# Performance work log

Hardware: AMD Instinct MI355X
Metric: run time of the kernel (lower is better)

Reference implementation:

```python
import jax, jax.numpy as jnp
import numpy as np

C_IN = 2048
N_EXP = 64
TOPK = 2


def setup_inputs() -> dict:
    key = jax.random.key(0)
    kx, kw, kb = jax.random.split(key, 3)
    x = jax.random.normal(kx, (4, 4096, C_IN), dtype=jnp.float32)
    # nn.Linear(c_in, n_exp): weight [n_exp, c_in], bias [n_exp]
    bound = 1.0 / np.sqrt(C_IN)
    W = jax.random.uniform(kw, (N_EXP, C_IN), minval=-bound, maxval=bound, dtype=jnp.float32)
    b = jax.random.uniform(kb, (N_EXP,), minval=-bound, maxval=bound, dtype=jnp.float32)
    return {"x": x, "W": W, "b": b}


def reference(x, W, b):
    # linear: [B,S,C] @ [C,E] + [E] -> [B,S,E]
    logits = jnp.einsum("bsc,ec->bse", x, W) + b
    probs = jax.nn.softmax(logits, axis=-1)
    vals, idx = jax.lax.top_k(probs, TOPK)  # [B,S,K]
    # scatter top-k values back to full expert dim; other entries zero
    onehot = jax.nn.one_hot(idx, N_EXP, dtype=probs.dtype)  # [B,S,K,E]
    gate_out = jnp.einsum("bsk,bske->bse", vals, onehot)
    return gate_out
```

## Files before the change

kernel.cpp:

```cpp
#include <hip/hip_runtime.h>
#include <math.h>

#define C_IN 2048
#define N_EXP 64
#define TPB 16
#define KWIN 512
#define KSTEPS 16
#define DELTA  3e-4f
#define DELTA2 1e-3f

typedef __bf16 bf16x8 __attribute__((ext_vector_type(8)));
typedef float f32x4 __attribute__((ext_vector_type(4)));

__device__ __forceinline__ void cvt_split(float f, ushort& h, ushort& l) {
    uint u = __float_as_uint(f);
    uint hr = (u + (0x7FFFu + ((u >> 16) & 1u))) >> 16;
    h = (ushort)hr;
    float hf = __uint_as_float(hr << 16);
    uint v = __float_as_uint(f - hf);
    l = (ushort)((v + (0x7FFFu + ((v >> 16) & 1u))) >> 16);
}

__global__ void conv_w_kernel(const float* __restrict__ W,
                              ushort* __restrict__ whf, ushort* __restrict__ wlf) {
    const int o = blockIdx.x * 256 + threadIdx.x;
    const int egks = o >> 9;
    const int lane = (o >> 3) & 63;
    const int j = o & 7;
    const int e = (egks >> 6) * 16 + (lane & 15);
    const int k = (egks & 63) * 32 + (lane >> 4) * 8 + j;
    ushort h, lo;
    cvt_split(W[e * C_IN + k], h, lo);
    whf[o] = h;
    wlf[o] = lo;
}

__global__ __launch_bounds__(256, 4) void topk_gate_kernel(
    const float* __restrict__ x, const float* __restrict__ Wf,
    const float* __restrict__ b, const ushort* __restrict__ whf,
    const ushort* __restrict__ wlf, float* __restrict__ out)
{
    __shared__ float part[4][TPB][65];

    const int tid = threadIdx.x;
    const int wv = tid >> 6, l = tid & 63;
    const int t0 = blockIdx.x * TPB;
    const int tr = l & 15;
    const int kg = l >> 4;

    const float* xg = x + (size_t)(t0 + tr) * C_IN + wv * KWIN + kg * 8;

    f32x4 acc[4];
#pragma unroll
    for (int eg = 0; eg < 4; ++eg) acc[eg] = (f32x4){0.f, 0.f, 0.f, 0.f};

#pragma unroll 2
    for (int ks = 0; ks < KSTEPS; ++ks) {
        const float4 a0 = *(const float4*)(xg + ks * 32);
        const float4 a1 = *(const float4*)(xg + ks * 32 + 4);
        const int ksa = wv * KSTEPS + ks;
        uint4 wb[8];
#pragma unroll
        for (int eg = 0; eg < 4; ++eg) {
            wb[eg * 2 + 0] = *(const uint4*)&whf[(eg * 64 + ksa) * 512 + l * 8];
            wb[eg * 2 + 1] = *(const uint4*)&wlf[(eg * 64 + ksa) * 512 + l * 8];
        }
        ushort h[8], q[8];
        cvt_split(a0.x, h[0], q[0]); cvt_split(a0.y, h[1], q[1]);
        cvt_split(a0.z, h[2], q[2]); cvt_split(a0.w, h[3], q[3]);
        cvt_split(a1.x, h[4], q[4]); cvt_split(a1.y, h[5], q[5]);
        cvt_split(a1.z, h[6], q[6]); cvt_split(a1.w, h[7], q[7]);
        uint4 hv = {(uint)h[0] | ((uint)h[1] << 16), (uint)h[2] | ((uint)h[3] << 16),
                    (uint)h[4] | ((uint)h[5] << 16), (uint)h[6] | ((uint)h[7] << 16)};
        uint4 qv = {(uint)q[0] | ((uint)q[1] << 16), (uint)q[2] | ((uint)q[3] << 16),
                    (uint)q[4] | ((uint)q[5] << 16), (uint)q[6] | ((uint)q[7] << 16)};
        bf16x8 ah = __builtin_bit_cast(bf16x8, hv);
        bf16x8 al = __builtin_bit_cast(bf16x8, qv);
#pragma unroll
        for (int eg = 0; eg < 4; ++eg) {
            bf16x8 bh = __builtin_bit_cast(bf16x8, wb[eg * 2 + 0]);
            bf16x8 bl = __builtin_bit_cast(bf16x8, wb[eg * 2 + 1]);
            acc[eg] = __builtin_amdgcn_mfma_f32_16x16x32_bf16(ah, bh, acc[eg], 0, 0, 0);
            acc[eg] = __builtin_amdgcn_mfma_f32_16x16x32_bf16(al, bh, acc[eg], 0, 0, 0);
            acc[eg] = __builtin_amdgcn_mfma_f32_16x16x32_bf16(ah, bl, acc[eg], 0, 0, 0);
        }
    }

#pragma unroll
    for (int eg = 0; eg < 4; ++eg)
#pragma unroll
    for (int r = 0; r < 4; ++r)
        part[wv][kg * 4 + r][eg * 16 + tr] = acc[eg][r];
    __syncthreads();

    const int e = l;
    const float be = b[e];
    for (int ti = 0; ti < 4; ++ti) {
        const int t = wv * 4 + ti;
        float logit = part[0][t][e] + part[1][t][e]
                    + part[2][t][e] + part[3][t][e] + be;

        float v1, v2, v3; int i1, i2;
        for (int pass = 0; pass < 2; ++pass) {
            v1 = logit; i1 = e;
#pragma unroll
            for (int off = 32; off >= 1; off >>= 1) {
                float ov = __shfl_xor(v1, off, 64);
                int   oi = __shfl_xor(i1, off, 64);
                if (ov > v1 || (ov == v1 && oi < i1)) { v1 = ov; i1 = oi; }
            }
            v2 = (e == i1) ? -3.4e38f : logit;
            i2 = (e == i1) ? N_EXP : e;
#pragma unroll
            for (int off = 32; off >= 1; off >>= 1) {
                float ov = __shfl_xor(v2, off, 64);
                int   oi = __shfl_xor(i2, off, 64);
                if (ov > v2 || (ov == v2 && oi < i2)) { v2 = ov; i2 = oi; }
            }
            v3 = (e == i1 || e == i2) ? -3.4e38f : logit;
#pragma unroll
            for (int off = 32; off >= 1; off >>= 1) {
                float ov = __shfl_xor(v3, off, 64);
                v3 = (ov > v3) ? ov : v3;
            }
            if (pass == 1) break;
            const bool risky = (v1 - v2 < DELTA) || (v2 - v3 < DELTA);
            if (!risky) break;
            unsigned long long cm = __ballot(logit >= v2 - DELTA2);
            const float* xr = x + (size_t)(t0 + t) * C_IN;
            while (cm) {
                const int ce = __ffsll((unsigned long long)cm) - 1;
                cm &= cm - 1;
                const float* wr = Wf + (size_t)ce * C_IN;
                float p = 0.f;
#pragma unroll 8
                for (int i = 0; i < 32; ++i)
                    p = fmaf(xr[l + 64 * i], wr[l + 64 * i], p);
#pragma unroll
                for (int off = 32; off >= 1; off >>= 1)
                    p += __shfl_xor(p, off, 64);
                if (e == ce) logit = p + be;
            }
        }

        float ex = expf(logit - v1);
        float ssum = ex;
#pragma unroll
        for (int off = 32; off >= 1; off >>= 1)
            ssum += __shfl_xor(ssum, off, 64);
        const float inv = 1.0f / ssum;
        const float p1 = inv;
        const float p2 = expf(v2 - v1) * inv;
        const float o = (e == i1) ? p1 : ((e == i2) ? p2 : 0.0f);
        out[(size_t)(t0 + t) * N_EXP + e] = o;
    }
}

extern "C" void kernel_launch(void* const* d_in, const int* in_sizes, int n_in,
                              void* d_out, int out_size, void* d_ws, size_t ws_size,
                              hipStream_t stream) {
    const float* x = (const float*)d_in[0];
    const float* W = (const float*)d_in[1];
    const float* b = (const float*)d_in[2];
    float* out = (float*)d_out;

    ushort* whf = (ushort*)d_ws;
    ushort* wlf = whf + N_EXP * C_IN;

    conv_w_kernel<<<512, 256, 0, stream>>>(W, whf, wlf);

    const int tokens = in_sizes[0] / C_IN;
    const int grid = tokens / TPB;
    topk_gate_kernel<<<grid, 256, 0, stream>>>(x, W, b, whf, wlf, out);
}
```

Baseline: 56.47 us.

## Double-buffer weight tiles via async global-to-LDS loads and process 32 tokens per block

Each block now handles 32 tokens as two 16-row MFMA fragments, so every weight fragment loaded is reused across twice as many tokens. Weight tiles are streamed into double-buffered LDS with global_load_lds while the next x chunk is prefetched into registers, and explicit vmcnt waits overlap loads with the MFMA work. MFMA issue priority is raised around the compute section. This lowers weight traffic per token and hides load latency, at the cost of 64KB of LDS per block, lower occupancy (launch bounds 2) and half as many blocks.

```diff
diff --git a/kernel.cpp b/kernel.cpp
--- a/kernel.cpp
+++ b/kernel.cpp
@@ -3,8 +3,7 @@
 
 #define C_IN 2048
 #define N_EXP 64
-#define TPB 16
-#define KWIN 512
+#define TPB 32
 #define KSTEPS 16
 #define DELTA  3e-4f
 #define DELTA2 1e-3f
@@ -35,70 +34,131 @@
     wlf[o] = lo;
 }
 
-__global__ __launch_bounds__(256, 4) void topk_gate_kernel(
+__device__ __forceinline__ void gload16(const ushort* g, ushort* l) {
+    __builtin_amdgcn_global_load_lds(
+        (const __attribute__((address_space(1))) uint32_t*)g,
+        (__attribute__((address_space(3))) uint32_t*)l, 16, 0, 0);
+}
+
+__global__ __launch_bounds__(256, 2) void topk_gate_kernel(
     const float* __restrict__ x, const float* __restrict__ Wf,
     const float* __restrict__ b, const ushort* __restrict__ whf,
     const ushort* __restrict__ wlf, float* __restrict__ out)
 {
-    __shared__ float part[4][TPB][65];
+    __shared__ __align__(16) ushort smem[32768];
 
     const int tid = threadIdx.x;
-    const int wv = tid >> 6, l = tid & 63;
+    const int w = tid >> 6, l = tid & 63;
     const int t0 = blockIdx.x * TPB;
     const int tr = l & 15;
     const int kg = l >> 4;
 
-    const float* xg = x + (size_t)(t0 + tr) * C_IN + wv * KWIN + kg * 8;
-
-    f32x4 acc[4];
-#pragma unroll
-    for (int eg = 0; eg < 4; ++eg) acc[eg] = (f32x4){0.f, 0.f, 0.f, 0.f};
-
-#pragma unroll 2
-    for (int ks = 0; ks < KSTEPS; ++ks) {
-        const float4 a0 = *(const float4*)(xg + ks * 32);
-        const float4 a1 = *(const float4*)(xg + ks * 32 + 4);
-        const int ksa = wv * KSTEPS + ks;
-        uint4 wb[8];
+    ushort* wbase = smem + w * 8192;
+
+    const float* xg = x + (size_t)t0 * C_IN + w * (KSTEPS * 32) + kg * 8;
+
+    f32x4 acc[2][4];
+#pragma unroll
+    for (int mf = 0; mf < 2; ++mf)
+#pragma unroll
+    for (int eg = 0; eg < 4; ++eg) acc[mf][eg] = (f32x4){0.f, 0.f, 0.f, 0.f};
+
+#define WSTAGE(I) do {                                                        \
+    const int ksa_ = w * KSTEPS + (I);                                        \
+    ushort* dst_ = wbase + ((I) & 1) * 4096;                                  \
+    _Pragma("unroll") for (int eg_ = 0; eg_ < 4; ++eg_) {                     \
+        gload16(whf + (size_t)(eg_ * 64 + ksa_) * 512 + l * 8,                \
+                dst_ + (eg_ * 2 + 0) * 512 + l * 8);                          \
+        gload16(wlf + (size_t)(eg_ * 64 + ksa_) * 512 + l * 8,                \
+                dst_ + (eg_ * 2 + 1) * 512 + l * 8);                          \
+    } } while (0)
+
+#define XLOAD(DST, I) do {                                                    \
+    (DST)[0] = *(const float4*)(xg + (size_t)tr * C_IN + (I) * 32);           \
+    (DST)[1] = *(const float4*)(xg + (size_t)tr * C_IN + (I) * 32 + 4);       \
+    (DST)[2] = *(const float4*)(xg + (size_t)(tr + 16) * C_IN + (I) * 32);    \
+    (DST)[3] = *(const float4*)(xg + (size_t)(tr + 16) * C_IN + (I) * 32 + 4);\
+    } while (0)
+
+    float4 xb[2][4];
+    WSTAGE(0);
+    XLOAD(xb[0], 0);
+
+#pragma unroll
+    for (int i = 0; i < KSTEPS; ++i) {
+        if (i + 1 < KSTEPS) {
+            WSTAGE(i + 1);
+            XLOAD(xb[(i + 1) & 1], i + 1);
+            asm volatile("s_waitcnt vmcnt(12)" ::: "memory");
+        } else {
+            asm volatile("s_waitcnt vmcnt(0)" ::: "memory");
+        }
+        __builtin_amdgcn_sched_barrier(0);
+
+        const ushort* tb = wbase + (i & 1) * 4096;
+        uint4 bfr[8];
 #pragma unroll
         for (int eg = 0; eg < 4; ++eg) {
-            wb[eg * 2 + 0] = *(const uint4*)&whf[(eg * 64 + ksa) * 512 + l * 8];
-            wb[eg * 2 + 1] = *(const uint4*)&wlf[(eg * 64 + ksa) * 512 + l * 8];
-        }
-        ushort h[8], q[8];
-        cvt_split(a0.x, h[0], q[0]); cvt_split(a0.y, h[1], q[1]);
-        cvt_split(a0.z, h[2], q[2]); cvt_split(a0.w, h[3], q[3]);
-        cvt_split(a1.x, h[4], q[4]); cvt_split(a1.y, h[5], q[5]);
-        cvt_split(a1.z, h[6], q[6]); cvt_split(a1.w, h[7], q[7]);
-        uint4 hv = {(uint)h[0] | ((uint)h[1] << 16), (uint)h[2] | ((uint)h[3] << 16),
+            bfr[eg * 2 + 0] = *(const uint4*)&tb[(eg * 2 + 0) * 512 + l * 8];
+            bfr[eg * 2 + 1] = *(const uint4*)&tb[(eg * 2 + 1) * 512 + l * 8];
+        }
+
+        const float4* xc = xb[i & 1];
+        ushort h[16], q[16];
+        cvt_split(xc[0].x, h[0], q[0]); cvt_split(xc[0].y, h[1], q[1]);
+        cvt_split(xc[0].z, h[2], q[2]); cvt_split(xc[0].w, h[3], q[3]);
+        cvt_split(xc[1].x, h[4], q[4]); cvt_split(xc[1].y, h[5], q[5]);
+        cvt_split(xc[1].z, h[6], q[6]); cvt_split(xc[1].w, h[7], q[7]);
+        cvt_split(xc[2].x, h[8], q[8]); cvt_split(xc[2].y, h[9], q[9]);
+        cvt_split(xc[2].z, h[10], q[10]); cvt_split(xc[2].w, h[11], q[11]);
+        cvt_split(xc[3].x, h[12], q[12]); cvt_split(xc[3].y, h[13], q[13]);
+        cvt_split(xc[3].z, h[14], q[14]); cvt_split(xc[3].w, h[15], q[15]);
+        uint4 h0 = {(uint)h[0] | ((uint)h[1] << 16), (uint)h[2] | ((uint)h[3] << 16),
                     (uint)h[4] | ((uint)h[5] << 16), (uint)h[6] | ((uint)h[7] << 16)};
-        uint4 qv = {(uint)q[0] | ((uint)q[1] << 16), (uint)q[2] | ((uint)q[3] << 16),
+        uint4 q0 = {(uint)q[0] | ((uint)q[1] << 16), (uint)q[2] | ((uint)q[3] << 16),
                     (uint)q[4] | ((uint)q[5] << 16), (uint)q[6] | ((uint)q[7] << 16)};
-        bf16x8 ah = __builtin_bit_cast(bf16x8, hv);
-        bf16x8 al = __builtin_bit_cast(bf16x8, qv);
+        uint4 h1 = {(uint)h[8] | ((uint)h[9] << 16), (uint)h[10] | ((uint)h[11] << 16),
+                    (uint)h[12] | ((uint)h[13] << 16), (uint)h[14] | ((uint)h[15] << 16)};
+        uint4 q1 = {(uint)q[8] | ((uint)q[9] << 16), (uint)q[10] | ((uint)q[11] << 16),
+                    (uint)q[12] | ((uint)q[13] << 16), (uint)q[14] | ((uint)q[15] << 16)};
+        bf16x8 ah0 = __builtin_bit_cast(bf16x8, h0);
+        bf16x8 al0 = __builtin_bit_cast(bf16x8, q0);
+        bf16x8 ah1 = __builtin_bit_cast(bf16x8, h1);
+        bf16x8 al1 = __builtin_bit_cast(bf16x8, q1);
+
+        __builtin_amdgcn_s_setprio(1);
 #pragma unroll
         for (int eg = 0; eg < 4; ++eg) {
-            bf16x8 bh = __builtin_bit_cast(bf16x8, wb[eg * 2 + 0]);
-            bf16x8 bl = __builtin_bit_cast(bf16x8, wb[eg * 2 + 1]);
-            acc[eg] = __builtin_amdgcn_mfma_f32_16x16x32_bf16(ah, bh, acc[eg], 0, 0, 0);
-            acc[eg] = __builtin_amdgcn_mfma_f32_16x16x32_bf16(al, bh, acc[eg], 0, 0, 0);
-            acc[eg] = __builtin_amdgcn_mfma_f32_16x16x32_bf16(ah, bl, acc[eg], 0, 0, 0);
-        }
+            bf16x8 bh = __builtin_bit_cast(bf16x8, bfr[eg * 2 + 0]);
+            bf16x8 bl = __builtin_bit_cast(bf16x8, bfr[eg * 2 + 1]);
+            acc[0][eg] = __builtin_amdgcn_mfma_f32_16x16x32_bf16(ah0, bh, acc[0][eg], 0, 0, 0);
+            acc[1][eg] = __builtin_amdgcn_mfma_f32_16x16x32_bf16(ah1, bh, acc[1][eg], 0, 0, 0);
+            acc[0][eg] = __builtin_amdgcn_mfma_f32_16x16x32_bf16(al0, bh, acc[0][eg], 0, 0, 0);
+            acc[1][eg] = __builtin_amdgcn_mfma_f32_16x16x32_bf16(al1, bh, acc[1][eg], 0, 0, 0);
+            acc[0][eg] = __builtin_amdgcn_mfma_f32_16x16x32_bf16(ah0, bl, acc[0][eg], 0, 0, 0);
+            acc[1][eg] = __builtin_amdgcn_mfma_f32_16x16x32_bf16(ah1, bl, acc[1][eg], 0, 0, 0);
+        }
+        __builtin_amdgcn_s_setprio(0);
     }
 
+    float* pw = (float*)wbase;
+#pragma unroll
+    for (int mf = 0; mf < 2; ++mf)
 #pragma unroll
     for (int eg = 0; eg < 4; ++eg)
 #pragma unroll
     for (int r = 0; r < 4; ++r)
-        part[wv][kg * 4 + r][eg * 16 + tr] = acc[eg][r];
+        pw[(mf * 16 + kg * 4 + r) * 64 + eg * 16 + tr] = acc[mf][eg][r];
+
     __syncthreads();
 
+    const float* fp = (const float*)smem;
     const int e = l;
     const float be = b[e];
-    for (int ti = 0; ti < 4; ++ti) {
-        const int t = wv * 4 + ti;
-        float logit = part[0][t][e] + part[1][t][e]
-                    + part[2][t][e] + part[3][t][e] + be;
+    for (int ti = 0; ti < 8; ++ti) {
+        const int t = w * 8 + ti;
+        float logit = fp[0 * 4096 + t * 64 + e] + fp[1 * 4096 + t * 64 + e]
+                    + fp[2 * 4096 + t * 64 + e] + fp[3 * 4096 + t * 64 + e] + be;
 
         float v1, v2, v3; int i1, i2;
         for (int pass = 0; pass < 2; ++pass) {
@@ -154,6 +214,8 @@
         const float o = (e == i1) ? p1 : ((e == i2) ? p2 : 0.0f);
         out[(size_t)(t0 + t) * N_EXP + e] = o;
     }
+#undef WSTAGE
+#undef XLOAD
 }
 
 extern "C" void kernel_launch(void* const* d_in, const int* in_sizes, int n_in,
```

After: 54.59 us. -3.3%, faster.

## Stage weight and activation chunks through LDS with a 4-deep async pipeline

Applied to the files above, without the earlier changes.

Rewrites the gate GEMM so each block handles 32 tokens and the four waves split the expert dimension instead of K. Weight chunks are streamed into LDS with global_load_lds, and x chunks are converted to bf16 hi/lo once per block into LDS, both in a 4-stage ring with explicit vmcnt waits and barriers. This removes the cross-wave K-reduction and cuts redundant per-wave weight loads, in exchange for more barriers, lower occupancy (launch bounds 2) and fragile hand-tuned wait counts.

```diff
diff --git a/kernel.cpp b/kernel.cpp
--- a/kernel.cpp
+++ b/kernel.cpp
@@ -3,9 +3,8 @@
 
 #define C_IN 2048
 #define N_EXP 64
-#define TPB 16
-#define KWIN 512
-#define KSTEPS 16
+#define TPB 32
+#define NCH 64
 #define DELTA  3e-4f
 #define DELTA2 1e-3f
 
@@ -22,83 +21,143 @@
 }
 
 __global__ void conv_w_kernel(const float* __restrict__ W,
-                              ushort* __restrict__ whf, ushort* __restrict__ wlf) {
-    const int o = blockIdx.x * 256 + threadIdx.x;
-    const int egks = o >> 9;
-    const int lane = (o >> 3) & 63;
-    const int j = o & 7;
-    const int e = (egks >> 6) * 16 + (lane & 15);
-    const int k = (egks & 63) * 32 + (lane >> 4) * 8 + j;
+                              ushort* __restrict__ whc, ushort* __restrict__ wlc) {
+    const int i = blockIdx.x * 256 + threadIdx.x;
+    const int e = i >> 11, k = i & 2047;
+    const int o = (k >> 5) * 2048 + e * 32 + (k & 31);
     ushort h, lo;
-    cvt_split(W[e * C_IN + k], h, lo);
-    whf[o] = h;
-    wlf[o] = lo;
-}
-
-__global__ __launch_bounds__(256, 4) void topk_gate_kernel(
+    cvt_split(W[i], h, lo);
+    whc[o] = h;
+    wlc[o] = lo;
+}
+
+__device__ __forceinline__ void glds16(const ushort* g, ushort* l) {
+    __builtin_amdgcn_global_load_lds(
+        (const __attribute__((address_space(1))) uint32_t*)g,
+        (__attribute__((address_space(3))) uint32_t*)l, 16, 0, 0);
+}
+
+#define VMW(N) do { asm volatile("s_waitcnt vmcnt(" #N ")" ::: "memory");     \
+                    __builtin_amdgcn_sched_barrier(0); } while (0)
+
+#define CVTW(XV, S2) do {                                                     \
+    ushort h0_, h1_, h2_, h3_, q0_, q1_, q2_, q3_;                            \
+    cvt_split((XV).x, h0_, q0_); cvt_split((XV).y, h1_, q1_);                 \
+    cvt_split((XV).z, h2_, q2_); cvt_split((XV).w, h3_, q3_);                 \
+    uint2 hv_ = {(uint)h0_ | ((uint)h1_ << 16), (uint)h2_ | ((uint)h3_ << 16)}; \
+    uint2 lv_ = {(uint)q0_ | ((uint)q1_ << 16), (uint)q2_ | ((uint)q3_ << 16)}; \
+    *(uint2*)&smem[16384 + (S2) * 2048 + xw] = hv_;                           \
+    *(uint2*)&smem[16384 + (S2) * 2048 + 1024 + xw] = lv_;                    \
+} while (0)
+
+#define KSTEP(u, W1, STG, CVT, W2) do {                                       \
+    VMW(W1);                                                                  \
+    __builtin_amdgcn_s_barrier();                                             \
+    const ushort* xs_ = smem + 16384 + (u) * 2048;                            \
+    const ushort* ws_ = smem + (u) * 4096;                                    \
+    uint4 rah0 = *(const uint4*)&xs_[aoff];                                   \
+    uint4 rah1 = *(const uint4*)&xs_[512 + aoff];                             \
+    uint4 ral0 = *(const uint4*)&xs_[1024 + aoff];                            \
+    uint4 ral1 = *(const uint4*)&xs_[1536 + aoff];                            \
+    uint4 rbh  = *(const uint4*)&ws_[boff];                                   \
+    uint4 rbl  = *(const uint4*)&ws_[2048 + boff];                            \
+    asm volatile("s_waitcnt lgkmcnt(0)" ::: "memory");                        \
+    __builtin_amdgcn_sched_barrier(0);                                        \
+    __builtin_amdgcn_s_barrier();                                             \
+    if (STG) {                                                                \
+        const int c4_ = cc + (u) + 4;                                         \
+        glds16(whc + (size_t)c4_ * 2048 + tid * 8,                            \
+               smem + (u) * 4096 + wavebase);                                 \
+        glds16(wlc + (size_t)c4_ * 2048 + tid * 8,                            \
+               smem + (u) * 4096 + 2048 + wavebase);                          \
+        xr[u] = *(const float4*)(xg + (size_t)xrow * C_IN + c4_ * 32 + xq * 4); \
+        __builtin_amdgcn_sched_barrier(0);                                    \
+    }                                                                         \
+    __builtin_amdgcn_s_setprio(1);                                            \
+    {                                                                         \
+        bf16x8 ah0 = __builtin_bit_cast(bf16x8, rah0);                        \
+        bf16x8 ah1 = __builtin_bit_cast(bf16x8, rah1);                        \
+        bf16x8 al0 = __builtin_bit_cast(bf16x8, ral0);                        \
+        bf16x8 al1 = __builtin_bit_cast(bf16x8, ral1);                        \
+        bf16x8 bh = __builtin_bit_cast(bf16x8, rbh);                          \
+        bf16x8 bl = __builtin_bit_cast(bf16x8, rbl);                          \
+        acc0 = __builtin_amdgcn_mfma_f32_16x16x32_bf16(ah0, bh, acc0, 0, 0, 0); \
+        acc1 = __builtin_amdgcn_mfma_f32_16x16x32_bf16(ah1, bh, acc1, 0, 0, 0); \
+        acc0 = __builtin_amdgcn_mfma_f32_16x16x32_bf16(al0, bh, acc0, 0, 0, 0); \
+        acc1 = __builtin_amdgcn_mfma_f32_16x16x32_bf16(al1, bh, acc1, 0, 0, 0); \
+        acc0 = __builtin_amdgcn_mfma_f32_16x16x32_bf16(ah0, bl, acc0, 0, 0, 0); \
+        acc1 = __builtin_amdgcn_mfma_f32_16x16x32_bf16(ah1, bl, acc1, 0, 0, 0); \
+    }                                                                         \
+    __builtin_amdgcn_s_setprio(0);                                            \
+    if (CVT) {                                                                \
+        VMW(W2);                                                              \
+        CVTW(xr[((u) + 2) & 3], ((u) + 2) & 3);                               \
+    }                                                                         \
+} while (0)
+
+__global__ __launch_bounds__(256, 2) void topk_gate_kernel(
     const float* __restrict__ x, const float* __restrict__ Wf,
-    const float* __restrict__ b, const ushort* __restrict__ whf,
-    const ushort* __restrict__ wlf, float* __restrict__ out)
+    const float* __restrict__ b, const ushort* __restrict__ whc,
+    const ushort* __restrict__ wlc, float* __restrict__ out)
 {
-    __shared__ float part[4][TPB][65];
+    __shared__ __align__(16) ushort smem[24576];
 
     const int tid = threadIdx.x;
-    const int wv = tid >> 6, l = tid & 63;
+    const int w = tid >> 6, l = tid & 63;
+    const int tr = l & 15, kg = l >> 4;
+    const int xrow = tid >> 3, xq = tid & 7;
     const int t0 = blockIdx.x * TPB;
-    const int tr = l & 15;
-    const int kg = l >> 4;
-
-    const float* xg = x + (size_t)(t0 + tr) * C_IN + wv * KWIN + kg * 8;
-
-    f32x4 acc[4];
-#pragma unroll
-    for (int eg = 0; eg < 4; ++eg) acc[eg] = (f32x4){0.f, 0.f, 0.f, 0.f};
-
-#pragma unroll 2
-    for (int ks = 0; ks < KSTEPS; ++ks) {
-        const float4 a0 = *(const float4*)(xg + ks * 32);
-        const float4 a1 = *(const float4*)(xg + ks * 32 + 4);
-        const int ksa = wv * KSTEPS + ks;
-        uint4 wb[8];
-#pragma unroll
-        for (int eg = 0; eg < 4; ++eg) {
-            wb[eg * 2 + 0] = *(const uint4*)&whf[(eg * 64 + ksa) * 512 + l * 8];
-            wb[eg * 2 + 1] = *(const uint4*)&wlf[(eg * 64 + ksa) * 512 + l * 8];
-        }
-        ushort h[8], q[8];
-        cvt_split(a0.x, h[0], q[0]); cvt_split(a0.y, h[1], q[1]);
-        cvt_split(a0.z, h[2], q[2]); cvt_split(a0.w, h[3], q[3]);
-        cvt_split(a1.x, h[4], q[4]); cvt_split(a1.y, h[5], q[5]);
-        cvt_split(a1.z, h[6], q[6]); cvt_split(a1.w, h[7], q[7]);
-        uint4 hv = {(uint)h[0] | ((uint)h[1] << 16), (uint)h[2] | ((uint)h[3] << 16),
-                    (uint)h[4] | ((uint)h[5] << 16), (uint)h[6] | ((uint)h[7] << 16)};
-        uint4 qv = {(uint)q[0] | ((uint)q[1] << 16), (uint)q[2] | ((uint)q[3] << 16),
-                    (uint)q[4] | ((uint)q[5] << 16), (uint)q[6] | ((uint)q[7] << 16)};
-        bf16x8 ah = __builtin_bit_cast(bf16x8, hv);
-        bf16x8 al = __builtin_bit_cast(bf16x8, qv);
-#pragma unroll
-        for (int eg = 0; eg < 4; ++eg) {
-            bf16x8 bh = __builtin_bit_cast(bf16x8, wb[eg * 2 + 0]);
-            bf16x8 bl = __builtin_bit_cast(bf16x8, wb[eg * 2 + 1]);
-            acc[eg] = __builtin_amdgcn_mfma_f32_16x16x32_bf16(ah, bh, acc[eg], 0, 0, 0);
-            acc[eg] = __builtin_amdgcn_mfma_f32_16x16x32_bf16(al, bh, acc[eg], 0, 0, 0);
-            acc[eg] = __builtin_amdgcn_mfma_f32_16x16x32_bf16(ah, bl, acc[eg], 0, 0, 0);
-        }
-    }
-
-#pragma unroll
-    for (int eg = 0; eg < 4; ++eg)
-#pragma unroll
-    for (int r = 0; r < 4; ++r)
-        part[wv][kg * 4 + r][eg * 16 + tr] = acc[eg][r];
+    const int wavebase = w * 512;
+    const int aoff = tr * 32 + kg * 8;
+    const int boff = (w * 16 + tr) * 32 + kg * 8;
+    const int xw = xrow * 32 + xq * 4;
+
+    const float* xg = x + (size_t)t0 * C_IN;
+
+    f32x4 acc0 = {0.f, 0.f, 0.f, 0.f};
+    f32x4 acc1 = {0.f, 0.f, 0.f, 0.f};
+    float4 xr[4];
+
+#pragma unroll
+    for (int c0 = 0; c0 < 4; ++c0) {
+        glds16(whc + (size_t)c0 * 2048 + tid * 8, smem + c0 * 4096 + wavebase);
+        glds16(wlc + (size_t)c0 * 2048 + tid * 8, smem + c0 * 4096 + 2048 + wavebase);
+        xr[c0] = *(const float4*)(xg + (size_t)xrow * C_IN + c0 * 32 + xq * 4);
+        __builtin_amdgcn_sched_barrier(0);
+    }
+    VMW(6);
+    CVTW(xr[0], 0);
+    CVTW(xr[1], 1);
+    asm volatile("s_waitcnt lgkmcnt(0)" ::: "memory");
+    __builtin_amdgcn_sched_barrier(0);
+
+    int cc = 0;
+#pragma unroll 1
+    for (int j = 0; j < 15; ++j) {
+        KSTEP(0, 9, 1, 1, 6);
+        KSTEP(1, 9, 1, 1, 6);
+        KSTEP(2, 9, 1, 1, 6);
+        KSTEP(3, 9, 1, 1, 6);
+        cc += 4;
+    }
+    KSTEP(0, 9, 0, 1, 3);
+    KSTEP(1, 6, 0, 1, 0);
+    KSTEP(2, 3, 0, 0, 0);
+    KSTEP(3, 0, 0, 0, 0);
+
+    float* part = (float*)smem;
+#pragma unroll
+    for (int r = 0; r < 4; ++r) {
+        part[(kg * 4 + r) * 65 + w * 16 + tr] = acc0[r];
+        part[(16 + kg * 4 + r) * 65 + w * 16 + tr] = acc1[r];
+    }
     __syncthreads();
 
     const int e = l;
     const float be = b[e];
-    for (int ti = 0; ti < 4; ++ti) {
-        const int t = wv * 4 + ti;
-        float logit = part[0][t][e] + part[1][t][e]
-                    + part[2][t][e] + part[3][t][e] + be;
+    for (int ti = 0; ti < 8; ++ti) {
+        const int t = w * 8 + ti;
+        float logit = part[t * 65 + e] + be;
 
         float v1, v2, v3; int i1, i2;
         for (int pass = 0; pass < 2; ++pass) {
@@ -127,7 +186,7 @@
             const bool risky = (v1 - v2 < DELTA) || (v2 - v3 < DELTA);
             if (!risky) break;
             unsigned long long cm = __ballot(logit >= v2 - DELTA2);
-            const float* xr = x + (size_t)(t0 + t) * C_IN;
+            const float* xrp = x + (size_t)(t0 + t) * C_IN;
             while (cm) {
                 const int ce = __ffsll((unsigned long long)cm) - 1;
                 cm &= cm - 1;
@@ -135,7 +194,7 @@
                 float p = 0.f;
 #pragma unroll 8
                 for (int i = 0; i < 32; ++i)
-                    p = fmaf(xr[l + 64 * i], wr[l + 64 * i], p);
+                    p = fmaf(xrp[l + 64 * i], wr[l + 64 * i], p);
 #pragma unroll
                 for (int off = 32; off >= 1; off >>= 1)
                     p += __shfl_xor(p, off, 64);
@@ -164,12 +223,12 @@
     const float* b = (const float*)d_in[2];
     float* out = (float*)d_out;
 
-    ushort* whf = (ushort*)d_ws;
-    ushort* wlf = whf + N_EXP * C_IN;
-
-    conv_w_kernel<<<512, 256, 0, stream>>>(W, whf, wlf);
+    ushort* whc = (ushort*)d_ws;
+    ushort* wlc = whc + N_EXP * C_IN;
+
+    conv_w_kernel<<<512, 256, 0, stream>>>(W, whc, wlc);
 
     const int tokens = in_sizes[0] / C_IN;
     const int grid = tokens / TPB;
-    topk_gate_kernel<<<grid, 256, 0, stream>>>(x, W, b, whf, wlf, out);
-}
+    topk_gate_kernel<<<grid, 256, 0, stream>>>(x, W, b, whc, wlc, out);
+}
```

After: 66.03 us. 16.9% more time.

## Stage x and split weights through LDS with async global-to-LDS pipelining

Applied to the files above, without the earlier changes.

The GEMM is restructured so each block handles 32 tokens and each wave owns 16 experts across the full K dimension, instead of splitting K across waves and reducing partials afterwards. x tiles (swizzled) and per-wave weight fragments are streamed into LDS with global_load_lds, double/quad buffered, with explicit vmcnt waits and barriers. The goal is to overlap memory loads with MFMA work, share x across waves and drop the cross-wave partial reduction. In exchange, 64KB of LDS limits occupancy to 2 blocks per CU, and the hand-scheduled wait counts are fragile.

```diff
diff --git a/kernel.cpp b/kernel.cpp
--- a/kernel.cpp
+++ b/kernel.cpp
@@ -3,9 +3,8 @@
 
 #define C_IN 2048
 #define N_EXP 64
-#define TPB 16
-#define KWIN 512
-#define KSTEPS 16
+#define TPB 32
+#define NSC 16
 #define DELTA  3e-4f
 #define DELTA2 1e-3f
 
@@ -24,81 +23,156 @@
 __global__ void conv_w_kernel(const float* __restrict__ W,
                               ushort* __restrict__ whf, ushort* __restrict__ wlf) {
     const int o = blockIdx.x * 256 + threadIdx.x;
-    const int egks = o >> 9;
-    const int lane = (o >> 3) & 63;
+    const int wg = o >> 15;
+    const int ks = (o >> 9) & 63;
+    const int l = (o >> 3) & 63;
     const int j = o & 7;
-    const int e = (egks >> 6) * 16 + (lane & 15);
-    const int k = (egks & 63) * 32 + (lane >> 4) * 8 + j;
+    const int e = wg * 16 + (l & 15);
+    const int k = ks * 32 + (l >> 4) * 8 + j;
     ushort h, lo;
     cvt_split(W[e * C_IN + k], h, lo);
     whf[o] = h;
     wlf[o] = lo;
 }
 
-__global__ __launch_bounds__(256, 4) void topk_gate_kernel(
+__device__ __forceinline__ void glds16(const void* g, void* l) {
+    __builtin_amdgcn_global_load_lds(
+        (const __attribute__((address_space(1))) uint32_t*)g,
+        (__attribute__((address_space(3))) uint32_t*)l, 16, 0, 0);
+}
+
+__device__ __forceinline__ void cvt8(const float4 a, const float4 b2,
+                                     uint4& hv, uint4& lv) {
+    ushort h[8], q[8];
+    cvt_split(a.x, h[0], q[0]);  cvt_split(a.y, h[1], q[1]);
+    cvt_split(a.z, h[2], q[2]);  cvt_split(a.w, h[3], q[3]);
+    cvt_split(b2.x, h[4], q[4]); cvt_split(b2.y, h[5], q[5]);
+    cvt_split(b2.z, h[6], q[6]); cvt_split(b2.w, h[7], q[7]);
+    hv = (uint4){(uint)h[0] | ((uint)h[1] << 16), (uint)h[2] | ((uint)h[3] << 16),
+                 (uint)h[4] | ((uint)h[5] << 16), (uint)h[6] | ((uint)h[7] << 16)};
+    lv = (uint4){(uint)q[0] | ((uint)q[1] << 16), (uint)q[2] | ((uint)q[3] << 16),
+                 (uint)q[4] | ((uint)q[5] << 16), (uint)q[6] | ((uint)q[7] << 16)};
+}
+
+#define VMW(N) do { asm volatile("s_waitcnt vmcnt(" #N ")" ::: "memory");     \
+                    __builtin_amdgcn_sched_barrier(0); } while (0)
+
+#define STAGEX(BB, SCN) do {                                                  \
+    char* xd_ = smem + (BB) * 16384;                                          \
+    _Pragma("unroll") for (int i_ = 0; i_ < 4; ++i_) {                        \
+        const int row0_ = w * 8 + 2 * i_;                                     \
+        const int r_ = row0_ + (l >> 5);                                      \
+        const int su_ = (l & 31) ^ ((r_ & 7) << 1);                           \
+        glds16((const float*)x + (size_t)(t0 + r_) * C_IN + (SCN) * 128 + su_ * 4, \
+               (float*)(xd_ + row0_ * 512));                                  \
+    }                                                                         \
+    __builtin_amdgcn_sched_barrier(0);                                        \
+} while (0)
+
+#define KSTEP(K, VMN, DOSTG) do {                                             \
+    if (DOSTG) {                                                              \
+        const int ksg2_ = sc4 + (K) + 2;                                      \
+        const size_t wo_ = ((size_t)(w * 64 + ksg2_)) * 512 + l * 8;          \
+        glds16(whf + wo_, wsl + (((K) + 2) & 3) * 2048);                      \
+        glds16(wlf + wo_, wsl + (((K) + 2) & 3) * 2048 + 1024);               \
+        __builtin_amdgcn_sched_barrier(0);                                    \
+    }                                                                         \
+    VMW(VMN);                                                                 \
+    {                                                                         \
+        const int uo_ = (((K) * 8 + kg2) ^ sw) * 16;                         \
+        float4 a0lo_ = *(const float4*)(xb + aoff0 + uo_);                    \
+        float4 a0hi_ = *(const float4*)(xb + aoff0 + uo_ + 16);               \
+        float4 a1lo_ = *(const float4*)(xb + aoff1 + uo_);                    \
+        float4 a1hi_ = *(const float4*)(xb + aoff1 + uo_ + 16);               \
+        uint4 bhu_ = *(const uint4*)(wsl + ((K) & 3) * 2048 + l * 16);        \
+        uint4 blu_ = *(const uint4*)(wsl + ((K) & 3) * 2048 + 1024 + l * 16); \
+        uint4 h0_, l0_, h1_, l1_;                                             \
+        cvt8(a0lo_, a0hi_, h0_, l0_);                                         \
+        cvt8(a1lo_, a1hi_, h1_, l1_);                                         \
+        bf16x8 ah0_ = __builtin_bit_cast(bf16x8, h0_);                        \
+        bf16x8 al0_ = __builtin_bit_cast(bf16x8, l0_);                        \
+        bf16x8 ah1_ = __builtin_bit_cast(bf16x8, h1_);                        \
+        bf16x8 al1_ = __builtin_bit_cast(bf16x8, l1_);                        \
+        bf16x8 bh_ = __builtin_bit_cast(bf16x8, bhu_);                        \
+        bf16x8 bl_ = __builtin_bit_cast(bf16x8, blu_);                        \
+        __builtin_amdgcn_s_setprio(1);                                        \
+        acc0 = __builtin_amdgcn_mfma_f32_16x16x32_bf16(ah0_, bh_, acc0, 0, 0, 0); \
+        acc1 = __builtin_amdgcn_mfma_f32_16x16x32_bf16(ah1_, bh_, acc1, 0, 0, 0); \
+        acc0 = __builtin_amdgcn_mfma_f32_16x16x32_bf16(al0_, bh_, acc0, 0, 0, 0); \
+        acc1 = __builtin_amdgcn_mfma_f32_16x16x32_bf16(al1_, bh_, acc1, 0, 0, 0); \
+        acc0 = __builtin_amdgcn_mfma_f32_16x16x32_bf16(ah0_, bl_, acc0, 0, 0, 0); \
+        acc1 = __builtin_amdgcn_mfma_f32_16x16x32_bf16(ah1_, bl_, acc1, 0, 0, 0); \
+        __builtin_amdgcn_s_setprio(0);                                        \
+    }                                                                         \
+} while (0)
+
+__global__ __launch_bounds__(256, 2) void topk_gate_kernel(
     const float* __restrict__ x, const float* __restrict__ Wf,
     const float* __restrict__ b, const ushort* __restrict__ whf,
     const ushort* __restrict__ wlf, float* __restrict__ out)
 {
-    __shared__ float part[4][TPB][65];
+    __shared__ __align__(16) char smem[65536];
 
     const int tid = threadIdx.x;
-    const int wv = tid >> 6, l = tid & 63;
+    const int w = tid >> 6, l = tid & 63;
+    const int tr = l & 15, kg = l >> 4;
+    const int kg2 = kg * 2;
+    const int sw = (tr & 7) << 1;
+    const int aoff0 = tr * 512;
+    const int aoff1 = (tr + 16) * 512;
     const int t0 = blockIdx.x * TPB;
-    const int tr = l & 15;
-    const int kg = l >> 4;
-
-    const float* xg = x + (size_t)(t0 + tr) * C_IN + wv * KWIN + kg * 8;
-
-    f32x4 acc[4];
-#pragma unroll
-    for (int eg = 0; eg < 4; ++eg) acc[eg] = (f32x4){0.f, 0.f, 0.f, 0.f};
-
-#pragma unroll 2
-    for (int ks = 0; ks < KSTEPS; ++ks) {
-        const float4 a0 = *(const float4*)(xg + ks * 32);
-        const float4 a1 = *(const float4*)(xg + ks * 32 + 4);
-        const int ksa = wv * KSTEPS + ks;
-        uint4 wb[8];
-#pragma unroll
-        for (int eg = 0; eg < 4; ++eg) {
-            wb[eg * 2 + 0] = *(const uint4*)&whf[(eg * 64 + ksa) * 512 + l * 8];
-            wb[eg * 2 + 1] = *(const uint4*)&wlf[(eg * 64 + ksa) * 512 + l * 8];
-        }
-        ushort h[8], q[8];
-        cvt_split(a0.x, h[0], q[0]); cvt_split(a0.y, h[1], q[1]);
-        cvt_split(a0.z, h[2], q[2]); cvt_split(a0.w, h[3], q[3]);
-        cvt_split(a1.x, h[4], q[4]); cvt_split(a1.y, h[5], q[5]);
-        cvt_split(a1.z, h[6], q[6]); cvt_split(a1.w, h[7], q[7]);
-        uint4 hv = {(uint)h[0] | ((uint)h[1] << 16), (uint)h[2] | ((uint)h[3] << 16),
-                    (uint)h[4] | ((uint)h[5] << 16), (uint)h[6] | ((uint)h[7] << 16)};
-        uint4 qv = {(uint)q[0] | ((uint)q[1] << 16), (uint)q[2] | ((uint)q[3] << 16),
-                    (uint)q[4] | ((uint)q[5] << 16), (uint)q[6] | ((uint)q[7] << 16)};
-        bf16x8 ah = __builtin_bit_cast(bf16x8, hv);
-        bf16x8 al = __builtin_bit_cast(bf16x8, qv);
-#pragma unroll
-        for (int eg = 0; eg < 4; ++eg) {
-            bf16x8 bh = __builtin_bit_cast(bf16x8, wb[eg * 2 + 0]);
-            bf16x8 bl = __builtin_bit_cast(bf16x8, wb[eg * 2 + 1]);
-            acc[eg] = __builtin_amdgcn_mfma_f32_16x16x32_bf16(ah, bh, acc[eg], 0, 0, 0);
-            acc[eg] = __builtin_amdgcn_mfma_f32_16x16x32_bf16(al, bh, acc[eg], 0, 0, 0);
-            acc[eg] = __builtin_amdgcn_mfma_f32_16x16x32_bf16(ah, bl, acc[eg], 0, 0, 0);
-        }
-    }
-
-#pragma unroll
-    for (int eg = 0; eg < 4; ++eg)
-#pragma unroll
-    for (int r = 0; r < 4; ++r)
-        part[wv][kg * 4 + r][eg * 16 + tr] = acc[eg][r];
+    char* wsl = smem + 32768 + w * 8192;
+
+    f32x4 acc0 = {0.f, 0.f, 0.f, 0.f};
+    f32x4 acc1 = {0.f, 0.f, 0.f, 0.f};
+
+    STAGEX(0, 0);
+    {
+        const size_t wo0 = ((size_t)(w * 64 + 0)) * 512 + l * 8;
+        glds16(whf + wo0, wsl + 0 * 2048);
+        glds16(wlf + wo0, wsl + 0 * 2048 + 1024);
+        const size_t wo1 = ((size_t)(w * 64 + 1)) * 512 + l * 8;
+        glds16(whf + wo1, wsl + 1 * 2048);
+        glds16(wlf + wo1, wsl + 1 * 2048 + 1024);
+        __builtin_amdgcn_sched_barrier(0);
+    }
+    VMW(4);
+    __builtin_amdgcn_s_barrier();
+
+    int sc4 = 0;
+#pragma unroll 1
+    for (int sc = 0; sc < NSC - 1; ++sc) {
+        const char* xb = smem + (sc & 1) * 16384;
+        STAGEX((sc + 1) & 1, sc + 1);
+        KSTEP(0, 8, 1);
+        KSTEP(1, 8, 1);
+        KSTEP(2, 4, 1);
+        KSTEP(3, 4, 1);
+        VMW(8);
+        __builtin_amdgcn_s_barrier();
+        sc4 += 4;
+    }
+    {
+        const char* xb = smem + 16384;
+        KSTEP(0, 4, 1);
+        KSTEP(1, 4, 1);
+        KSTEP(2, 2, 0);
+        KSTEP(3, 0, 0);
+    }
+
+    float* part = (float*)smem;
+#pragma unroll
+    for (int r = 0; r < 4; ++r) {
+        part[(kg * 4 + r) * 65 + w * 16 + tr] = acc0[r];
+        part[(16 + kg * 4 + r) * 65 + w * 16 + tr] = acc1[r];
+    }
     __syncthreads();
 
     const int e = l;
     const float be = b[e];
-    for (int ti = 0; ti < 4; ++ti) {
-        const int t = wv * 4 + ti;
-        float logit = part[0][t][e] + part[1][t][e]
-                    + part[2][t][e] + part[3][t][e] + be;
+    for (int ti = 0; ti < 8; ++ti) {
+        const int t = w * 8 + ti;
+        float logit = part[t * 65 + e] + be;
 
         float v1, v2, v3; int i1, i2;
         for (int pass = 0; pass < 2; ++pass) {
```

Result: slower. 88.17 us (+56.1%).
